# Kernel tuning notes

Measured on AMD Instinct MI355X. Metric: run time of the kernel, lower is better.

The kernel has to match this reference:

```python
import jax, jax.numpy as jnp
import numpy as np

B, N, C, H = 8, 1024, 768, 12
HD = C // H  # 64
SCALE = HD ** -0.5
T = 4
N_HALF = T // 2  # loop body with attention runs N_HALF times, V accumulates T times


def setup_inputs() -> dict:
    key = jax.random.key(0)
    ks = jax.random.split(key, 8)
    s = 0.02
    return {
        "x": jax.random.normal(ks[0], (B, N, C), jnp.float32),
        "Wqkv": jax.random.normal(ks[1], (3 * C, C), jnp.float32) * s,
        "Wfc1": jax.random.normal(ks[2], (HD, HD), jnp.float32) * s,
        "bfc1": jax.random.normal(ks[3], (HD,), jnp.float32) * s,
        "Wfc2": jax.random.normal(ks[4], (HD, HD), jnp.float32) * s,
        "bfc2": jax.random.normal(ks[5], (HD,), jnp.float32) * s,
        "Wproj": jax.random.normal(ks[6], (C, C), jnp.float32) * s,
        "bproj": jax.random.normal(ks[7], (C,), jnp.float32) * s,
    }


def reference(x, Wqkv, Wfc1, bfc1, Wfc2, bfc2, Wproj, bproj):
    b, n, c = x.shape
    # qkv projection (no bias), split into per-head q,k,v: [B,H,N,hd]
    qkv = (x @ Wqkv.T).reshape(b, n, 3, H, HD).transpose(2, 0, 3, 1, 4)
    q, k, v = qkv[0], qkv[1], qkv[2]
    # Loop body is stateless per timestep: first N_HALF steps each add the same
    # att_spk; all T steps add the same relu(v). Compute once, scale by counts.
    Q_spk = jax.nn.relu(q) @ Wfc1.T + bfc1  # [B,H,N,hd]
    K_spk = jax.nn.relu(k) @ Wfc2.T + bfc2  # [B,H,N,hd]
    att_spk = jax.nn.relu(jnp.einsum("bhqd,bhkd->bhqk", Q_spk, K_spk) * SCALE)
    att_rec = att_spk * float(N_HALF)   # accumulated over t < T/2
    V_rec = jax.nn.relu(v) * float(T)   # accumulated over all T steps
    att = jax.nn.softmax(att_rec, axis=-1)
    out = jnp.einsum("bhqk,bhkd->bhqd", att, V_rec)  # [B,H,N,hd]
    out = out.transpose(0, 2, 1, 3).reshape(b, n, c)
    return out @ Wproj.T + bproj
```

## Files before the change

### kernel.cpp

```cpp
#include <hip/hip_runtime.h>
#include <hip/hip_bf16.h>
#include <stdint.h>
#include <math.h>

#define BB   8
#define NN_  1024
#define CC   768
#define HH   12
#define HDD  64

typedef __attribute__((ext_vector_type(8))) short bf16x8;
typedef __attribute__((ext_vector_type(4))) float f32x4;
typedef __attribute__((ext_vector_type(16))) float f32x16;
typedef __attribute__((ext_vector_type(4))) float f32x4v;
typedef __attribute__((ext_vector_type(4))) unsigned short u16x4;

union FragU { unsigned int u[4]; bf16x8 b; };

__device__ __forceinline__ unsigned short f2bf(float f) {
    union { float f; unsigned int u; } v; v.f = f;
    unsigned int r = v.u + 0x7fffu + ((v.u >> 16) & 1u);
    return (unsigned short)(r >> 16);
}

#define CVTPK(d_, a_, b_) asm("v_cvt_pk_bf16_f32 %0, %1, %2" : "=v"(d_) : "v"(a_), "v"(b_))
#define SWAP32(a_, b_) asm("v_permlane32_swap_b32 %0, %1" : "+v"(a_), "+v"(b_))

#define GLDS(g_, l_) __builtin_amdgcn_global_load_lds( \
    (const __attribute__((address_space(1))) void*)(g_), \
    (__attribute__((address_space(3))) void*)(l_), 16, 0, 0)

#define MKFRAGS(P_, F0_, F1_) do {                                             \
    unsigned int c0,c1,c2,c3,c4,c5,c6,c7;                                      \
    CVTPK(c0, P_[0],  P_[1]);  CVTPK(c1, P_[2],  P_[3]);                       \
    CVTPK(c2, P_[4],  P_[5]);  CVTPK(c3, P_[6],  P_[7]);                       \
    CVTPK(c4, P_[8],  P_[9]);  CVTPK(c5, P_[10], P_[11]);                      \
    CVTPK(c6, P_[12], P_[13]); CVTPK(c7, P_[14], P_[15]);                      \
    SWAP32(c0, c2); SWAP32(c1, c3); SWAP32(c4, c6); SWAP32(c5, c7);            \
    FragU fu0_, fu1_;                                                          \
    fu0_.u[0]=c0; fu0_.u[1]=c1; fu0_.u[2]=c2; fu0_.u[3]=c3;                    \
    fu1_.u[0]=c4; fu1_.u[1]=c5; fu1_.u[2]=c6; fu1_.u[3]=c7;                    \
    F0_ = fu0_.b; F1_ = fu1_.b;                                                \
} while (0)

#define CVT_N0 1572864
#define CVT_N1 2015232
#define CVT_N2 2162688
#define CVT_N3 2163712
#define CVT_N4 2164736
__global__ void cvt_all(const float* __restrict__ x, const float* __restrict__ wqkv,
                        const float* __restrict__ wproj, const float* __restrict__ wf1,
                        const float* __restrict__ wf2,
                        unsigned short* __restrict__ xb, unsigned short* __restrict__ wqkvb,
                        unsigned short* __restrict__ wprojb, unsigned short* __restrict__ wf1b,
                        unsigned short* __restrict__ wf2b) {
    int i = blockIdx.x * blockDim.x + threadIdx.x;
    int stride = gridDim.x * blockDim.x;
    for (; i < CVT_N4; i += stride) {
        const f32x4v* src; u16x4* dst; int off;
        if (i < CVT_N0)      { src = (const f32x4v*)x;     dst = (u16x4*)xb;     off = i; }
        else if (i < CVT_N1) { src = (const f32x4v*)wqkv;  dst = (u16x4*)wqkvb;  off = i - CVT_N0; }
        else if (i < CVT_N2) { src = (const f32x4v*)wproj; dst = (u16x4*)wprojb; off = i - CVT_N1; }
        else if (i < CVT_N3) { src = (const f32x4v*)wf1;   dst = (u16x4*)wf1b;   off = i - CVT_N2; }
        else                 { src = (const f32x4v*)wf2;   dst = (u16x4*)wf2b;   off = i - CVT_N3; }
        f32x4v v = src[off];
        u16x4 o;
        o.x = f2bf(v.x); o.y = f2bf(v.y); o.z = f2bf(v.z); o.w = f2bf(v.w);
        dst[off] = o;
    }
}

__global__ __launch_bounds__(512, 1)
void qkv_spk_gemm(const unsigned short* __restrict__ X,
                  const unsigned short* __restrict__ Wqkv,
                  const unsigned short* __restrict__ Wf1,
                  const unsigned short* __restrict__ Wf2,
                  const float* __restrict__ bf1,
                  const float* __restrict__ bf2,
                  unsigned short* __restrict__ Rq,
                  unsigned short* __restrict__ Rk,
                  unsigned short* __restrict__ VT) {
    __shared__ short sA[4][8192];
    __shared__ short sB[4][4096];

    const int t    = threadIdx.x;
    const int wid  = t >> 6;
    const int lane = t & 63;
    const int l31  = lane & 31;
    const int hi5  = lane >> 5;
    const int fw   = wid >> 1;
    const int wn   = wid & 1;

    const int bid  = (int)blockIdx.x;
    const int c    = bid & 7;
    const int j    = bid >> 3;
    const int f_   = j % 9;
    const int g_   = j / 9;
    const int bx   = c * 8 + g_;
    const int by   = f_;
    const int F0   = by * 256;
    const int T0   = bx * 128;

#define STG(bi_, kt_) do {                                                     \
    _Pragma("unroll")                                                          \
    for (int i = 0; i < 2; i++) {                                              \
        int li_ = i * 512 + t;                                                 \
        int dr_ = li_ >> 3;                                                    \
        int u_  = (li_ & 7) ^ (dr_ & 7);                                       \
        GLDS(Wqkv + (size_t)(F0 + dr_ * 2 + (u_ >> 2)) * 768 + (kt_) * 32 + (u_ & 3) * 8, \
             &sA[bi_][li_ * 8]);                                               \
    }                                                                          \
    {                                                                          \
        int dr_ = t >> 3;                                                      \
        int u_  = (t & 7) ^ (dr_ & 7);                                         \
        GLDS(X + (size_t)(T0 + dr_ * 2 + (u_ >> 2)) * 768 + (kt_) * 32 + (u_ & 3) * 8, \
             &sB[bi_][t * 8]);                                                 \
    }                                                                          \
} while (0)

    f32x16 acc[2][2];
#pragma unroll
    for (int fb = 0; fb < 2; fb++)
#pragma unroll
        for (int tb = 0; tb < 2; tb++)
#pragma unroll
            for (int r = 0; r < 16; r++) acc[fb][tb][r] = 0.f;

    bf16x8 wA[2][2], xA[2][2], wB[2][2], xB[2][2];

#define RD(W_, X_, bc_) do {                                                   \
    const char* ab_ = (const char*)sA[bc_];                                    \
    const char* bb_ = (const char*)sB[bc_];                                    \
    _Pragma("unroll")                                                          \
    for (int fb = 0; fb < 2; fb++) {                                           \
        int r_ = fw * 64 + fb * 32 + l31;                                      \
        int dr_ = r_ >> 1;                                                     \
        _Pragma("unroll")                                                      \
        for (int ks = 0; ks < 2; ks++)                                         \
            W_[fb][ks] = *(const bf16x8*)(ab_ + dr_ * 128 +                    \
                ((((r_ & 1) * 4 + ks * 2 + hi5) ^ (dr_ & 7)) << 4));           \
    }                                                                          \
    _Pragma("unroll")                                                          \
    for (int tb = 0; tb < 2; tb++) {                                           \
        int r_ = wn * 64 + tb * 32 + l31;                                      \
        int dr_ = r_ >> 1;                                                     \
        _Pragma("unroll")                                                      \
        for (int ks = 0; ks < 2; ks++)                                         \
            X_[tb][ks] = *(const bf16x8*)(bb_ + dr_ * 128 +                    \
                ((((r_ & 1) * 4 + ks * 2 + hi5) ^ (dr_ & 7)) << 4));           \
    }                                                                          \
} while (0)

#define MFMA8(W_, X_)                                                          \
    _Pragma("unroll")                                                          \
    for (int ks = 0; ks < 2; ks++)                                             \
        _Pragma("unroll")                                                      \
        for (int fb = 0; fb < 2; fb++)                                         \
            _Pragma("unroll")                                                  \
            for (int tb = 0; tb < 2; tb++)                                     \
                acc[fb][tb] = __builtin_amdgcn_mfma_f32_32x32x16_bf16(         \
                    W_[fb][ks], X_[tb][ks], acc[fb][tb], 0, 0, 0)

#define PH(CW_, CX_, NW_, NX_, rb_, sb_, t_, VM_) do {                         \
    if ((t_) + 3 < 24) STG(sb_, (t_) + 3);                                     \
    asm volatile("s_waitcnt vmcnt(" #VM_ ")" ::: "memory");                    \
    __builtin_amdgcn_s_barrier();                                              \
    if ((t_) + 1 < 24) RD(NW_, NX_, rb_);                                      \
    __builtin_amdgcn_sched_barrier(0);                                         \
    __builtin_amdgcn_s_setprio(1);                                             \
    MFMA8(CW_, CX_);                                                           \
    __builtin_amdgcn_s_setprio(0);                                             \
    asm volatile("s_waitcnt lgkmcnt(0)" ::: "memory");                         \
} while (0)

    STG(0, 0); STG(1, 1); STG(2, 2);
    asm volatile("s_waitcnt vmcnt(6)" ::: "memory");
    __builtin_amdgcn_s_barrier();
    RD(wA, xA, 0);
    asm volatile("s_waitcnt lgkmcnt(0)" ::: "memory");

#pragma unroll 1
    for (int t4 = 0; t4 < 20; t4 += 4) {
        PH(wA, xA, wB, xB, 1, 3, t4 + 0, 6);
        PH(wB, xB, wA, xA, 2, 0, t4 + 1, 6);
        PH(wA, xA, wB, xB, 3, 1, t4 + 2, 6);
        PH(wB, xB, wA, xA, 0, 2, t4 + 3, 6);
    }
    PH(wA, xA, wB, xB, 1, 3, 20, 6);
    PH(wB, xB, wA, xA, 2, 0, 21, 3);
    PH(wA, xA, wB, xB, 3, 1, 22, 0);
    PH(wB, xB, wA, xA, 0, 2, 23, 0);
#undef PH
#undef MFMA8
#undef RD
#undef STG

    const int fbase = F0 + fw * 64;
    const int p  = fbase / 768;
    const int hh = (fbase - p * 768) >> 6;
    const int tok0 = T0 + wn * 64;
    const int b  = tok0 >> 10;
    const int n0 = tok0 & 1023;
    const int crow0 = 4 * hi5;

    if (p == 2) {
        const size_t vtb = ((size_t)(b * HH + hh)) * HDD * NN_;
#pragma unroll
        for (int fb = 0; fb < 2; fb++)
#pragma unroll
            for (int tb = 0; tb < 2; tb++)
#pragma unroll
                for (int r = 0; r < 16; r++) {
                    int d = fb * 32 + (r & 3) + 8 * (r >> 2) + crow0;
                    int n = n0 + tb * 32 + l31;
                    VT[vtb + (size_t)d * NN_ + n] = f2bf(4.f * fmaxf(acc[fb][tb][r], 0.f));
                }
    } else {
        const unsigned short* Wf = p ? Wf2 : Wf1;
        const float* bfp = p ? bf2 : bf1;
        unsigned short* R = p ? Rk : Rq;
        bf16x8 wfr[2][4];
#pragma unroll
        for (int dh = 0; dh < 2; dh++)
#pragma unroll
            for (int ks = 0; ks < 4; ks++)
                wfr[dh][ks] = *(const bf16x8*)&Wf[(size_t)(dh * 32 + l31) * HDD + ks * 16 + hi5 * 8];
        float bv0 = bfp[l31], bv1 = bfp[32 + l31];
        const size_t qkb = ((size_t)(b * HH + hh)) * NN_ * HDD;
#pragma unroll
        for (int tb = 0; tb < 2; tb++) {
            float pv0[16], pv1[16];
#pragma unroll
            for (int r = 0; r < 16; r++) {
                pv0[r] = fmaxf(acc[0][tb][r], 0.f);
                pv1[r] = fmaxf(acc[1][tb][r], 0.f);
            }
            bf16x8 pa0, pa1, pa2, pa3;
            MKFRAGS(pv0, pa0, pa1);
            MKFRAGS(pv1, pa2, pa3);
            f32x16 D0, D1;
#pragma unroll
            for (int r = 0; r < 16; r++) { D0[r] = 0.f; D1[r] = 0.f; }
            D0 = __builtin_amdgcn_mfma_f32_32x32x16_bf16(pa0, wfr[0][0], D0, 0, 0, 0);
            D0 = __builtin_amdgcn_mfma_f32_32x32x16_bf16(pa1, wfr[0][1], D0, 0, 0, 0);
            D0 = __builtin_amdgcn_mfma_f32_32x32x16_bf16(pa2, wfr[0][2], D0, 0, 0, 0);
            D0 = __builtin_amdgcn_mfma_f32_32x32x16_bf16(pa3, wfr[0][3], D0, 0, 0, 0);
            D1 = __builtin_amdgcn_mfma_f32_32x32x16_bf16(pa0, wfr[1][0], D1, 0, 0, 0);
            D1 = __builtin_amdgcn_mfma_f32_32x32x16_bf16(pa1, wfr[1][1], D1, 0, 0, 0);
            D1 = __builtin_amdgcn_mfma_f32_32x32x16_bf16(pa2, wfr[1][2], D1, 0, 0, 0);
            D1 = __builtin_amdgcn_mfma_f32_32x32x16_bf16(pa3, wfr[1][3], D1, 0, 0, 0);
#pragma unroll
            for (int r = 0; r < 16; r++) {
                int n = n0 + tb * 32 + (r & 3) + 8 * (r >> 2) + crow0;
                size_t rowb = qkb + (size_t)n * HDD;
                R[rowb + l31]      = f2bf(D0[r] + bv0);
                R[rowb + 32 + l31] = f2bf(D1[r] + bv1);
            }
        }
    }
}

__global__ __launch_bounds__(256, 2)
void attn_kernel(const unsigned short* __restrict__ Q,
                 const unsigned short* __restrict__ Kx,
                 const unsigned short* __restrict__ VT,
                 unsigned short* __restrict__ AO) {
    __shared__ short sK[3][4096];
    __shared__ short sV[3][4096];
    __shared__ float sinv[4][32];

    const int t    = threadIdx.x;
    const int lane = t & 63;
    const int wid  = t >> 6;
    const int l31  = lane & 31;
    const int hi5  = lane >> 5;

    const int bid = (int)blockIdx.x;
    const int lbid = (bid & 7) * 96 + (bid >> 3);
    const int bh = lbid >> 3;
    const int qt = lbid & 7;
    const int b = bh / HH, h = bh - b * HH;

    const unsigned short* Qs = Q  + (size_t)bh * NN_ * HDD;
    const unsigned short* Ks = Kx + (size_t)bh * NN_ * HDD;
    const unsigned short* Vt = VT + (size_t)bh * HDD * NN_;
    const int q0 = qt * 128 + wid * 32;

    bf16x8 qf[4];
#pragma unroll
    for (int ds = 0; ds < 4; ds++)
        qf[ds] = *(const bf16x8*)&Qs[(size_t)(q0 + l31) * HDD + ds * 16 + hi5 * 8];

    f32x16 O0, O1;
#pragma unroll
    for (int r = 0; r < 16; r++) { O0[r] = 0.f; O1[r] = 0.f; }
    float sumacc = 0.f;

    const int srow = t >> 3;
    const int sslot = t & 7;
    const int dstoff = ((t & 192)) * 8;

#define STAGE(buf_, kt_) do {                                                  \
    _Pragma("unroll")                                                          \
    for (int i = 0; i < 2; i++) {                                              \
        int row_ = srow + i * 32;                                              \
        int sl_  = (sslot ^ (row_ & 7)) << 3;                                  \
        const unsigned short* gk_ = Ks + (size_t)((kt_) * 64 + row_) * HDD + sl_; \
        const unsigned short* gv_ = Vt + (size_t)row_ * NN_ + (kt_) * 64 + sl_;   \
        GLDS(gk_, &sK[buf_][i * 2048 + dstoff]);                               \
        GLDS(gv_, &sV[buf_][i * 2048 + dstoff]);                               \
    }                                                                          \
} while (0)

#define ABODY(cb_, sb_, kt_, VM_) do {                                         \
    if ((kt_) + 2 < 16) STAGE(sb_, (kt_) + 2);                                 \
    const char* kbase = (const char*)&sK[cb_][0];                              \
    const char* vbase = (const char*)&sV[cb_][0];                              \
    bf16x8 vbf[4][2];                                                          \
    _Pragma("unroll")                                                          \
    for (int ks = 0; ks < 4; ks++)                                             \
        _Pragma("unroll")                                                      \
        for (int dt = 0; dt < 2; dt++) {                                       \
            int d = dt * 32 + l31;                                             \
            vbf[ks][dt] = *(const bf16x8*)(vbase + d * 128 +                   \
                           ((ks * 32 + hi5 * 16) ^ ((d & 7) << 4)));           \
        }                                                                      \
    bf16x8 ka[2][4];                                                           \
    _Pragma("unroll")                                                          \
    for (int kt2 = 0; kt2 < 2; kt2++)                                          \
        _Pragma("unroll")                                                      \
        for (int ds = 0; ds < 4; ds++) {                                       \
            int kk = kt2 * 32 + l31;                                           \
            ka[kt2][ds] = *(const bf16x8*)(kbase + kk * 128 +                  \
                           ((ds * 32 + hi5 * 16) ^ ((kk & 7) << 4)));          \
        }                                                                      \
    f32x16 S0, S1;                                                             \
    _Pragma("unroll")                                                          \
    for (int r = 0; r < 16; r++) { S0[r] = 0.f; S1[r] = 0.f; }                 \
    _Pragma("unroll")                                                          \
    for (int ds = 0; ds < 4; ds++) {                                           \
        S0 = __builtin_amdgcn_mfma_f32_32x32x16_bf16(ka[0][ds], qf[ds], S0, 0, 0, 0); \
        S1 = __builtin_amdgcn_mfma_f32_32x32x16_bf16(ka[1][ds], qf[ds], S1, 0, 0, 0); \
    }                                                                          \
    float p0[16], p1[16];                                                      \
    _Pragma("unroll")                                                          \
    for (int r = 0; r < 16; r++) {                                             \
        p0[r] = exp2f(0.36067376f * fmaxf(S0[r], 0.f));                        \
        p1[r] = exp2f(0.36067376f * fmaxf(S1[r], 0.f));                        \
    }                                                                          \
    float s0 = 0.f, s1 = 0.f;                                                  \
    _Pragma("unroll")                                                          \
    for (int r = 0; r < 16; r++) { s0 += p0[r]; s1 += p1[r]; }                 \
    sumacc += s0 + s1;                                                         \
    bf16x8 paf0, paf1, paf2, paf3;                                             \
    MKFRAGS(p0, paf0, paf1);                                                   \
    MKFRAGS(p1, paf2, paf3);                                                   \
    O0 = __builtin_amdgcn_mfma_f32_32x32x16_bf16(paf0, vbf[0][0], O0, 0, 0, 0);\
    O1 = __builtin_amdgcn_mfma_f32_32x32x16_bf16(paf0, vbf[0][1], O1, 0, 0, 0);\
    O0 = __builtin_amdgcn_mfma_f32_32x32x16_bf16(paf1, vbf[1][0], O0, 0, 0, 0);\
    O1 = __builtin_amdgcn_mfma_f32_32x32x16_bf16(paf1, vbf[1][1], O1, 0, 0, 0);\
    O0 = __builtin_amdgcn_mfma_f32_32x32x16_bf16(paf2, vbf[2][0], O0, 0, 0, 0);\
    O1 = __builtin_amdgcn_mfma_f32_32x32x16_bf16(paf2, vbf[2][1], O1, 0, 0, 0);\
    O0 = __builtin_amdgcn_mfma_f32_32x32x16_bf16(paf3, vbf[3][0], O0, 0, 0, 0);\
    O1 = __builtin_amdgcn_mfma_f32_32x32x16_bf16(paf3, vbf[3][1], O1, 0, 0, 0);\
    asm volatile("s_waitcnt vmcnt(" #VM_ ")" ::: "memory");                    \
    __builtin_amdgcn_s_barrier();                                              \
} while (0)

    STAGE(0, 0); STAGE(1, 1);
    asm volatile("s_waitcnt vmcnt(4)" ::: "memory");
    __builtin_amdgcn_s_barrier();

#pragma unroll 1
    for (int kt3 = 0; kt3 < 12; kt3 += 3) {
        ABODY(0, 2, kt3 + 0, 4);
        ABODY(1, 0, kt3 + 1, 4);
        ABODY(2, 1, kt3 + 2, 4);
    }
    ABODY(0, 2, 12, 4);
    ABODY(1, 0, 13, 4);
    ABODY(2, 1, 14, 0);
    ABODY(0, 2, 15, 0);
#undef ABODY
#undef STAGE

    float stot = sumacc + __shfl_xor(sumacc, 32, 64);
    float inv = 1.f / stot;
    if (l31 == lane) sinv[wid][l31] = inv;
    __syncthreads();

#pragma unroll
    for (int r = 0; r < 16; r++) {
        int qloc = (r & 3) + 8 * (r >> 2) + 4 * hi5;
        float iv = sinv[wid][qloc];
        size_t row = (size_t)(b * NN_ + q0 + qloc) * CC + h * HDD;
        AO[row + l31]      = f2bf(O0[r] * iv);
        AO[row + 32 + l31] = f2bf(O1[r] * iv);
    }
}

__global__ __launch_bounds__(256)
void proj_gemm(const unsigned short* __restrict__ A,
               const unsigned short* __restrict__ Bt,
               const float* __restrict__ bias,
               float* __restrict__ Out) {
    __shared__ short sA[3][4096];
    __shared__ short sB[3][4096];
    const int K = 768;
    const int lane = threadIdx.x & 63;
    const int wid  = threadIdx.x >> 6;
    const int wr = wid >> 1, wc = wid & 1;
    const int brow = blockIdx.x * 128;
    const int bcol = blockIdx.y * 128;
    const int t = threadIdx.x;

    f32x4 acc[4][4];
#pragma unroll
    for (int m = 0; m < 4; m++)
#pragma unroll
        for (int n = 0; n < 4; n++) acc[m][n] = (f32x4){0.f, 0.f, 0.f, 0.f};

#define PSTG(buf_, kt_) do {                                                   \
    _Pragma("unroll")                                                          \
    for (int i = 0; i < 2; i++) {                                              \
        int tt  = i * 256 + t;                                                 \
        int row = tt >> 2;                                                     \
        int kc  = (tt & 3) * 8;                                                \
        GLDS(A  + (size_t)(brow + row) * K + (kt_) * 32 + kc,                  \
             &sA[buf_][(i * 256 + wid * 64) * 8]);                             \
        GLDS(Bt + (size_t)(bcol + row) * K + (kt_) * 32 + kc,                  \
             &sB[buf_][(i * 256 + wid * 64) * 8]);                             \
    }                                                                          \
} while (0)

#define PBODY(cb_, sb_, kt_, VM_) do {                                         \
    if ((kt_) + 2 < 24) PSTG(sb_, (kt_) + 2);                                  \
    bf16x8 af[4], bfg[4];                                                      \
    _Pragma("unroll")                                                          \
    for (int m = 0; m < 4; m++) {                                              \
        int r = wr * 64 + m * 16 + (lane & 15);                                \
        af[m] = *(const bf16x8*)&sA[cb_][r * 32 + (lane >> 4) * 8];            \
    }                                                                          \
    _Pragma("unroll")                                                          \
    for (int n = 0; n < 4; n++) {                                              \
        int cc2 = wc * 64 + n * 16 + (lane & 15);                              \
        bfg[n] = *(const bf16x8*)&sB[cb_][cc2 * 32 + (lane >> 4) * 8];         \
    }                                                                          \
    _Pragma("unroll")                                                          \
    for (int m = 0; m < 4; m++)                                                \
        _Pragma("unroll")                                                      \
        for (int n = 0; n < 4; n++)                                            \
            acc[m][n] = __builtin_amdgcn_mfma_f32_16x16x32_bf16(af[m], bfg[n], acc[m][n], 0, 0, 0); \
    asm volatile("s_waitcnt vmcnt(" #VM_ ")" ::: "memory");                    \
    __builtin_amdgcn_s_barrier();                                              \
} while (0)

    PSTG(0, 0); PSTG(1, 1);
    asm volatile("s_waitcnt vmcnt(4)" ::: "memory");
    __builtin_amdgcn_s_barrier();

#pragma unroll 1
    for (int kt3 = 0; kt3 < 21; kt3 += 3) {
        PBODY(0, 2, kt3 + 0, 4);
        PBODY(1, 0, kt3 + 1, 4);
        PBODY(2, 1, kt3 + 2, 4);
    }
    PBODY(0, 2, 21, 4);
    PBODY(1, 0, 22, 0);
    PBODY(2, 1, 23, 0);
#undef PBODY
#undef PSTG

#pragma unroll
    for (int m = 0; m < 4; m++)
#pragma unroll
        for (int n = 0; n < 4; n++) {
            int col = bcol + wc * 64 + n * 16 + (lane & 15);
            float bv = bias[col];
#pragma unroll
            for (int r = 0; r < 4; r++) {
                int row = brow + wr * 64 + m * 16 + (lane >> 4) * 4 + r;
                Out[(size_t)row * 768 + col] = acc[m][n][r] + bv;
            }
        }
}

extern "C" void kernel_launch(void* const* d_in, const int* in_sizes, int n_in,
                              void* d_out, int out_size, void* d_ws, size_t ws_size,
                              hipStream_t stream) {
    const float* x     = (const float*)d_in[0];
    const float* Wqkv  = (const float*)d_in[1];
    const float* Wfc1  = (const float*)d_in[2];
    const float* bfc1  = (const float*)d_in[3];
    const float* Wfc2  = (const float*)d_in[4];
    const float* bfc2  = (const float*)d_in[5];
    const float* Wproj = (const float*)d_in[6];
    const float* bproj = (const float*)d_in[7];
    float* out = (float*)d_out;

    char* ws = (char*)d_ws;
    const size_t SZ_XN = (size_t)8192 * 768 * 2;
    unsigned short* x_bf    = (unsigned short*)ws; ws += SZ_XN;
    unsigned short* wqkv_bf = (unsigned short*)ws; ws += (size_t)2304 * 768 * 2;
    unsigned short* wproj_bf= (unsigned short*)ws; ws += (size_t)768 * 768 * 2;
    unsigned short* wfc1_bf = (unsigned short*)ws; ws += 64 * 64 * 2;
    unsigned short* wfc2_bf = (unsigned short*)ws; ws += 64 * 64 * 2;
    unsigned short* Rq      = (unsigned short*)ws; ws += SZ_XN;
    unsigned short* Rk      = (unsigned short*)ws; ws += SZ_XN;
    unsigned short* VT      = (unsigned short*)ws; ws += SZ_XN;

    cvt_all<<<2048, 256, 0, stream>>>(x, Wqkv, Wproj, Wfc1, Wfc2,
                                      x_bf, wqkv_bf, wproj_bf, wfc1_bf, wfc2_bf);
    qkv_spk_gemm<<<576, 512, 0, stream>>>(x_bf, wqkv_bf, wfc1_bf, wfc2_bf,
                                          bfc1, bfc2, Rq, Rk, VT);
    attn_kernel<<<768, 256, 0, stream>>>(Rq, Rk, VT, x_bf);
    proj_gemm<<<dim3(64, 6), 256, 0, stream>>>(x_bf, wproj_bf, bproj, out);
}
```

Baseline: 133.1 us.

## Shrink QKV and projection GEMM tiles to raise block count and occupancy

The QKV GEMM tile changes from 256x128 with 512 threads to 192x128 with 384 threads. That gives 768 blocks with launch bounds allowing 3 blocks per CU, and the X staging is split so 128 threads load the remaining rows. The projection GEMM tile shrinks from 128x128 to 128x64, launched as a 1D grid of 768 blocks with XCD-aware swizzled indexing and adjusted vmcnt waits. The goal is to fill all CUs better and balance waves across the chip, at the cost of lower per-block data reuse and more redundant loads. The hidden 254-line body of the QKV kernel is assumed to already depend on the wave layout (6 waves instead of 8), which cannot be verified.

```diff
diff --git a/kernel.cpp b/kernel.cpp
--- a/kernel.cpp
+++ b/kernel.cpp
@@ -70,7 +70,7 @@
     }
 }
 
-__global__ __launch_bounds__(512, 1)
+__global__ __launch_bounds__(384, 3)
 void qkv_spk_gemm(const unsigned short* __restrict__ X,
                   const unsigned short* __restrict__ Wqkv,
                   const unsigned short* __restrict__ Wf1,
@@ -80,7 +80,7 @@
                   unsigned short* __restrict__ Rq,
                   unsigned short* __restrict__ Rk,
                   unsigned short* __restrict__ VT) {
-    __shared__ short sA[4][8192];
+    __shared__ short sA[4][6144];
     __shared__ short sB[4][4096];
 
     const int t    = threadIdx.x;
@@ -94,17 +94,15 @@
     const int bid  = (int)blockIdx.x;
     const int c    = bid & 7;
     const int j    = bid >> 3;
-    const int f_   = j % 9;
-    const int g_   = j / 9;
-    const int bx   = c * 8 + g_;
-    const int by   = f_;
-    const int F0   = by * 256;
-    const int T0   = bx * 128;
+    const int f_   = j % 12;
+    const int g_   = j / 12;
+    const int F0   = f_ * 192;
+    const int T0   = (c * 8 + g_) * 128;
 
 #define STG(bi_, kt_) do {                                                     \
     _Pragma("unroll")                                                          \
     for (int i = 0; i < 2; i++) {                                              \
-        int li_ = i * 512 + t;                                                 \
+        int li_ = i * 384 + t;                                                 \
         int dr_ = li_ >> 3;                                                    \
         int u_  = (li_ & 7) ^ (dr_ & 7);                                       \
         GLDS(Wqkv + (size_t)(F0 + dr_ * 2 + (u_ >> 2)) * 768 + (kt_) * 32 + (u_ & 3) * 8, \
@@ -115,6 +113,13 @@
         int u_  = (t & 7) ^ (dr_ & 7);                                         \
         GLDS(X + (size_t)(T0 + dr_ * 2 + (u_ >> 2)) * 768 + (kt_) * 32 + (u_ & 3) * 8, \
              &sB[bi_][t * 8]);                                                 \
+    }                                                                          \
+    if (t < 128) {                                                             \
+        int li_ = 384 + t;                                                     \
+        int dr_ = li_ >> 3;                                                    \
+        int u_  = (li_ & 7) ^ (dr_ & 7);                                       \
+        GLDS(X + (size_t)(T0 + dr_ * 2 + (u_ >> 2)) * 768 + (kt_) * 32 + (u_ & 3) * 8, \
+             &sB[bi_][li_ * 8]);                                               \
     }                                                                          \
 } while (0)
 
@@ -405,67 +410,75 @@
                const float* __restrict__ bias,
                float* __restrict__ Out) {
     __shared__ short sA[3][4096];
-    __shared__ short sB[3][4096];
+    __shared__ short sB[3][2048];
     const int K = 768;
     const int lane = threadIdx.x & 63;
     const int wid  = threadIdx.x >> 6;
     const int wr = wid >> 1, wc = wid & 1;
-    const int brow = blockIdx.x * 128;
-    const int bcol = blockIdx.y * 128;
     const int t = threadIdx.x;
 
-    f32x4 acc[4][4];
+    const int bid = (int)blockIdx.x;
+    const int c   = bid & 7;
+    const int j   = bid >> 3;
+    const int brow = (c * 8 + j / 12) * 128;
+    const int bcol = (j % 12) * 64;
+
+    f32x4 acc[4][2];
 #pragma unroll
     for (int m = 0; m < 4; m++)
 #pragma unroll
-        for (int n = 0; n < 4; n++) acc[m][n] = (f32x4){0.f, 0.f, 0.f, 0.f};
+        for (int n = 0; n < 2; n++) acc[m][n] = (f32x4){0.f, 0.f, 0.f, 0.f};
 
 #define PSTG(buf_, kt_) do {                                                   \
     _Pragma("unroll")                                                          \
     for (int i = 0; i < 2; i++) {                                              \
-        int tt  = i * 256 + t;                                                 \
-        int row = tt >> 2;                                                     \
-        int kc  = (tt & 3) * 8;                                                \
-        GLDS(A  + (size_t)(brow + row) * K + (kt_) * 32 + kc,                  \
-             &sA[buf_][(i * 256 + wid * 64) * 8]);                             \
+        int li = i * 256 + t;                                                  \
+        int row = li >> 2;                                                     \
+        int kc  = (li & 3) * 8;                                                \
+        GLDS(A + (size_t)(brow + row) * K + (kt_) * 32 + kc,                   \
+             &sA[buf_][li * 8]);                                               \
+    }                                                                          \
+    {                                                                          \
+        int row = t >> 2;                                                      \
+        int kc  = (t & 3) * 8;                                                 \
         GLDS(Bt + (size_t)(bcol + row) * K + (kt_) * 32 + kc,                  \
-             &sB[buf_][(i * 256 + wid * 64) * 8]);                             \
+             &sB[buf_][t * 8]);                                                \
     }                                                                          \
 } while (0)
 
 #define PBODY(cb_, sb_, kt_, VM_) do {                                         \
     if ((kt_) + 2 < 24) PSTG(sb_, (kt_) + 2);                                  \
-    bf16x8 af[4], bfg[4];                                                      \
+    bf16x8 af[4], bfg[2];                                                      \
     _Pragma("unroll")                                                          \
     for (int m = 0; m < 4; m++) {                                              \
         int r = wr * 64 + m * 16 + (lane & 15);                                \
         af[m] = *(const bf16x8*)&sA[cb_][r * 32 + (lane >> 4) * 8];            \
     }                                                                          \
     _Pragma("unroll")                                                          \
-    for (int n = 0; n < 4; n++) {                                              \
-        int cc2 = wc * 64 + n * 16 + (lane & 15);                              \
+    for (int n = 0; n < 2; n++) {                                              \
+        int cc2 = wc * 32 + n * 16 + (lane & 15);                              \
         bfg[n] = *(const bf16x8*)&sB[cb_][cc2 * 32 + (lane >> 4) * 8];         \
     }                                                                          \
     _Pragma("unroll")                                                          \
     for (int m = 0; m < 4; m++)                                                \
         _Pragma("unroll")                                                      \
-        for (int n = 0; n < 4; n++)                                            \
+        for (int n = 0; n < 2; n++)                                            \
             acc[m][n] = __builtin_amdgcn_mfma_f32_16x16x32_bf16(af[m], bfg[n], acc[m][n], 0, 0, 0); \
     asm volatile("s_waitcnt vmcnt(" #VM_ ")" ::: "memory");                    \
     __builtin_amdgcn_s_barrier();                                              \
 } while (0)
 
     PSTG(0, 0); PSTG(1, 1);
-    asm volatile("s_waitcnt vmcnt(4)" ::: "memory");
+    asm volatile("s_waitcnt vmcnt(3)" ::: "memory");
     __builtin_amdgcn_s_barrier();
 
 #pragma unroll 1
     for (int kt3 = 0; kt3 < 21; kt3 += 3) {
-        PBODY(0, 2, kt3 + 0, 4);
-        PBODY(1, 0, kt3 + 1, 4);
-        PBODY(2, 1, kt3 + 2, 4);
+        PBODY(0, 2, kt3 + 0, 3);
+        PBODY(1, 0, kt3 + 1, 3);
+        PBODY(2, 1, kt3 + 2, 3);
     }
-    PBODY(0, 2, 21, 4);
+    PBODY(0, 2, 21, 3);
     PBODY(1, 0, 22, 0);
     PBODY(2, 1, 23, 0);
 #undef PBODY
@@ -474,8 +487,8 @@
 #pragma unroll
     for (int m = 0; m < 4; m++)
 #pragma unroll
-        for (int n = 0; n < 4; n++) {
-            int col = bcol + wc * 64 + n * 16 + (lane & 15);
+        for (int n = 0; n < 2; n++) {
+            int col = bcol + wc * 32 + n * 16 + (lane & 15);
             float bv = bias[col];
 #pragma unroll
             for (int r = 0; r < 4; r++) {
@@ -511,8 +524,8 @@
 
     cvt_all<<<2048, 256, 0, stream>>>(x, Wqkv, Wproj, Wfc1, Wfc2,
                                       x_bf, wqkv_bf, wproj_bf, wfc1_bf, wfc2_bf);
-    qkv_spk_gemm<<<576, 512, 0, stream>>>(x_bf, wqkv_bf, wfc1_bf, wfc2_bf,
+    qkv_spk_gemm<<<768, 384, 0, stream>>>(x_bf, wqkv_bf, wfc1_bf, wfc2_bf,
                                           bfc1, bfc2, Rq, Rk, VT);
     attn_kernel<<<768, 256, 0, stream>>>(Rq, Rk, VT, x_bf);
-    proj_gemm<<<dim3(64, 6), 256, 0, stream>>>(x_bf, wproj_bf, bproj, out);
+    proj_gemm<<<768, 256, 0, stream>>>(x_bf, wproj_bf, bproj, out);
 }
```

Result: no change. 133.9 us (+0.6%).
